# Performance work log

Measured on AMD Instinct MI355X. Metric: run time of the kernel, lower is better.

## Reference

```python
import jax, jax.numpy as jnp
import numpy as np

N_NODES = 100000
N_EDGES = 1600000
N_ETYPES = 3
IN_FEATS = 128
HEADS = 4
OUT_FEATS = 16
EDGE_FEATS = 64
NEG_SLOPE = 0.2


def setup_inputs() -> dict:
    key = jax.random.key(0)
    ks = jax.random.split(key, 10)
    return {
        "x": jax.random.normal(ks[0], (N_NODES, IN_FEATS), jnp.float32),
        "W": jax.random.normal(ks[1], (IN_FEATS, HEADS * OUT_FEATS), jnp.float32) * 0.05,
        "W_e": jax.random.normal(ks[2], (EDGE_FEATS, HEADS * EDGE_FEATS), jnp.float32) * 0.05,
        "attn_l": jax.random.normal(ks[3], (HEADS, OUT_FEATS), jnp.float32) * 0.1,
        "attn_r": jax.random.normal(ks[4], (HEADS, OUT_FEATS), jnp.float32) * 0.1,
        "attn_e": jax.random.normal(ks[5], (HEADS, EDGE_FEATS), jnp.float32) * 0.1,
        "edge_emb": jax.random.normal(ks[6], (N_ETYPES, EDGE_FEATS), jnp.float32),
        "src": jax.random.randint(ks[7], (N_EDGES,), 0, N_NODES, jnp.int32),
        "dst": jax.random.randint(ks[8], (N_EDGES,), 0, N_NODES, jnp.int32),
        "etype": jax.random.randint(ks[9], (N_EDGES,), 0, N_ETYPES, jnp.int32),
    }


def reference(x, W, W_e, attn_l, attn_r, attn_e, edge_emb, src, dst, etype):
    N = x.shape[0]
    H, D = attn_l.shape
    # node projection: [N, H, D]
    feat = (x @ W).reshape(N, H, D)
    # per-node attention halves: [N, H]
    el = jnp.einsum("nhd,hd->nh", feat, attn_l)
    er = jnp.einsum("nhd,hd->nh", feat, attn_r)
    # per-etype edge term: [T, H]
    e_feat = (edge_emb @ W_e).reshape(edge_emb.shape[0], H, -1)
    ee = jnp.einsum("the,he->th", e_feat, attn_e)
    # per-edge pre-softmax score: [E, H]
    s = el[src] + er[dst] + ee[etype]
    s = jnp.where(s > 0, s, NEG_SLOPE * s)  # leaky_relu
    # edge softmax over incoming edges of each dst node (homogeneous graph)
    m = jax.ops.segment_max(s, dst, num_segments=N)
    e = jnp.exp(s - m[dst])
    z = jax.ops.segment_sum(e, dst, num_segments=N)
    a = e / z[dst]  # [E, H]
    # u_mul_e + sum aggregation: [N, H, D]
    msg = feat[src] * a[:, :, None]
    rst = jax.ops.segment_sum(msg, dst, num_segments=N)
    return rst, a
```

## Files before the change

kernel.cpp:

```cpp
#include <hip/hip_runtime.h>
#include <hip/hip_bf16.h>

#define N_NODES   100000
#define N_EDGES   1600000
#define N_ETYPES  3
#define IN_FEATS  128
#define HEADS     4
#define OUT_FEATS 16
#define EDGE_FEATS 64
#define HD        64
#define NEG_SLOPE 0.2f
#define MAXD_LDS  128

#define NBUCK     800
#define NPB       125
#define PBLK      400
#define EPB       4000
#define BCAP      2560

typedef short s16x8 __attribute__((ext_vector_type(8)));
typedef float f32x4 __attribute__((ext_vector_type(4)));

__device__ __forceinline__ short f2bs(float f) {
    __hip_bfloat16 h = __float2bfloat16(f);
    return *reinterpret_cast<short*>(&h);
}

__global__ __launch_bounds__(256) void wt_prep_kernel(
    const float* __restrict__ W, short* __restrict__ WTb)
{
    const int t = blockIdx.x * 256 + threadIdx.x;
    const int k = t >> 6, n = t & 63;
    WTb[n * IN_FEATS + k] = f2bs(W[t]);
}

#define XS_STRIDE 136
__global__ __launch_bounds__(256) void feat_el_er_kernel(
    const float* __restrict__ x,
    const short* __restrict__ WTb,
    const float* __restrict__ attn_l,
    const float* __restrict__ attn_r,
    __hip_bfloat16* __restrict__ featb,
    float* __restrict__ el,
    float* __restrict__ er)
{
    __shared__ short Xs[16 * XS_STRIDE];
    __shared__ short Ws[64 * XS_STRIDE];

    const int t = threadIdx.x;
    const int row0 = blockIdx.x * 16;
    {
        const int r = t >> 4, k0 = (t & 15) * 8;
        const float4* xg = (const float4*)(x + (size_t)(row0 + r) * IN_FEATS + k0);
        const float4 v0 = xg[0], v1 = xg[1];
        s16x8 p;
        p[0] = f2bs(v0.x); p[1] = f2bs(v0.y); p[2] = f2bs(v0.z); p[3] = f2bs(v0.w);
        p[4] = f2bs(v1.x); p[5] = f2bs(v1.y); p[6] = f2bs(v1.z); p[7] = f2bs(v1.w);
        *(s16x8*)&Xs[r * XS_STRIDE + k0] = p;
    }
    {
#pragma unroll
        for (int j = 0; j < 4; ++j) {
            const int u = t + 256 * j;
            const int r = u >> 4, c = (u & 15) * 8;
            *(s16x8*)&Ws[r * XS_STRIDE + c] = *(const s16x8*)(WTb + r * IN_FEATS + c);
        }
    }
    __syncthreads();

    const int w    = t >> 6;
    const int lane = t & 63;
    const int m    = lane & 15;
    const int q    = lane >> 4;

    f32x4 acc = {0.f, 0.f, 0.f, 0.f};
#pragma unroll
    for (int kb = 0; kb < 4; ++kb) {
        const s16x8 af = *(const s16x8*)&Xs[m * XS_STRIDE + kb * 32 + q * 8];
        const s16x8 bf = *(const s16x8*)&Ws[(w * 16 + m) * XS_STRIDE + kb * 32 + q * 8];
        acc = __builtin_amdgcn_mfma_f32_16x16x32_bf16(af, bf, acc, 0, 0, 0);
    }

    const float al = attn_l[w * OUT_FEATS + m];
    const float ar = attn_r[w * OUT_FEATS + m];
#pragma unroll
    for (int r = 0; r < 4; ++r) {
        const int row = row0 + q * 4 + r;
        featb[(size_t)row * HD + w * 16 + m] = __float2bfloat16(acc[r]);
        float cl = acc[r] * al;
        float cr = acc[r] * ar;
#pragma unroll
        for (int msk = 1; msk < 16; msk <<= 1) {
            cl += __shfl_xor(cl, msk, 64);
            cr += __shfl_xor(cr, msk, 64);
        }
        if (m == 0) {
            el[row * HEADS + w] = cl;
            er[row * HEADS + w] = cr;
        }
    }
}

__global__ __launch_bounds__(64) void ee_kernel(
    const float* __restrict__ edge_emb,
    const float* __restrict__ W_e,
    const float* __restrict__ attn_e,
    float* __restrict__ ee)
{
    const int b  = blockIdx.x;
    const int ty = b >> 2;
    const int h  = b & 3;
    const int e  = threadIdx.x;

    float ef = 0.f;
#pragma unroll
    for (int k = 0; k < EDGE_FEATS; ++k)
        ef += edge_emb[ty * EDGE_FEATS + k] *
              W_e[k * (HEADS * EDGE_FEATS) + h * EDGE_FEATS + e];
    float v = ef * attn_e[h * EDGE_FEATS + e];
#pragma unroll
    for (int m = 1; m < 64; m <<= 1) v += __shfl_xor(v, m, 64);
    if (e == 0) ee[ty * HEADS + h] = v;
}

__global__ __launch_bounds__(256) void bucket_hist_kernel(
    const int* __restrict__ dst, int* __restrict__ bhist)
{
    __shared__ int h[NBUCK];
    const int t = threadIdx.x, b = blockIdx.x;
    for (int j = t; j < NBUCK; j += 256) h[j] = 0;
    __syncthreads();
    const int e0 = b * EPB;
    for (int i = t; i < EPB; i += 256)
        atomicAdd(&h[dst[e0 + i] / NPB], 1);
    __syncthreads();
    for (int j = t; j < NBUCK; j += 256) bhist[b * NBUCK + j] = h[j];
}

__global__ __launch_bounds__(256) void bucket_scan1_kernel(
    int* __restrict__ bhist, int* __restrict__ btot)
{
    __shared__ int sh[PBLK];
    const int t = threadIdx.x, j = blockIdx.x;
    const int j0 = t, j1 = t + 256;
    int o0 = 0, o1 = 0;
    if (j0 < PBLK) { o0 = bhist[j0 * NBUCK + j]; sh[j0] = o0; }
    if (j1 < PBLK) { o1 = bhist[j1 * NBUCK + j]; sh[j1] = o1; }
    __syncthreads();
    for (int off = 1; off < PBLK; off <<= 1) {
        int v0 = (j0 >= off && j0 < PBLK) ? sh[j0 - off] : 0;
        int v1 = (j1 >= off && j1 < PBLK) ? sh[j1 - off] : 0;
        __syncthreads();
        if (j0 < PBLK) sh[j0] += v0;
        if (j1 < PBLK) sh[j1] += v1;
        __syncthreads();
    }
    if (j0 < PBLK) bhist[j0 * NBUCK + j] = sh[j0] - o0;
    if (j1 < PBLK) bhist[j1 * NBUCK + j] = sh[j1] - o1;
    if (t == 255) btot[j] = sh[PBLK - 1];
}

__global__ __launch_bounds__(1024) void bucket_scan2_kernel(
    const int* __restrict__ btot, int* __restrict__ bbase)
{
    __shared__ int sh[NBUCK];
    const int t = threadIdx.x;
    int o = 0;
    if (t < NBUCK) { o = btot[t]; sh[t] = o; }
    __syncthreads();
    for (int off = 1; off < NBUCK; off <<= 1) {
        int v = (t >= off && t < NBUCK) ? sh[t - off] : 0;
        __syncthreads();
        if (t < NBUCK) sh[t] += v;
        __syncthreads();
    }
    if (t < NBUCK) bbase[t] = sh[t] - o;
    if (t == NBUCK - 1) bbase[NBUCK] = sh[t];
}

__global__ __launch_bounds__(256) void bucket_scatter_kernel(
    const int* __restrict__ src, const int* __restrict__ dst,
    const int* __restrict__ etype,
    const int* __restrict__ bhist, const int* __restrict__ bbase,
    int2* __restrict__ sc_bucket)
{
    __shared__ int cnt[NBUCK];
    const int t = threadIdx.x, b = blockIdx.x;
    for (int j = t; j < NBUCK; j += 256)
        cnt[j] = bbase[j] + bhist[b * NBUCK + j];
    __syncthreads();
    const int e0 = b * EPB;
    for (int i = t; i < EPB; i += 256) {
        const int e  = e0 + i;
        const int dn = dst[e];
        const int bu = dn / NPB;
        const int ld = dn - bu * NPB;
        const int slot = atomicAdd(&cnt[bu], 1);
        sc_bucket[slot] = make_int2(src[e], e | (etype[e] << 21) | (ld << 23));
    }
}

__global__ __launch_bounds__(256) void bucket_csr_kernel(
    const int2* __restrict__ sc_bucket, const int* __restrict__ bbase,
    int* __restrict__ ptr, int2* __restrict__ sc_csr)
{
    __shared__ int2 sbuf[BCAP];
    __shared__ int sdeg[128];
    __shared__ int scur[128];
    const int t = threadIdx.x, b = blockIdx.x;
    const int lo = bbase[b];
    const int count = bbase[b + 1] - lo;
    const bool staged = (count <= BCAP);

    if (t < 128) sdeg[t] = 0;
    __syncthreads();
    if (staged) {
        for (int i = t; i < count; i += 256) {
            const int2 v = sc_bucket[lo + i];
            sbuf[i] = v;
            atomicAdd(&sdeg[(v.y >> 23) & 0x7F], 1);
        }
    } else {
        for (int i = t; i < count; i += 256)
            atomicAdd(&sdeg[(sc_bucket[lo + i].y >> 23) & 0x7F], 1);
    }
    __syncthreads();
    const int orig = (t < 128) ? sdeg[t] : 0;
    for (int off = 1; off < 128; off <<= 1) {
        const int v = (t < 128 && t >= off) ? sdeg[t - off] : 0;
        __syncthreads();
        if (t < 128) sdeg[t] += v;
        __syncthreads();
    }
    if (t < 128) {
        const int excl = sdeg[t] - orig;
        if (t < NPB) ptr[b * NPB + t] = lo + excl;
        scur[t] = lo + excl;
    }
    if (b == 0 && t == 0) ptr[N_NODES] = N_EDGES;
    __syncthreads();
    if (staged) {
        for (int i = t; i < count; i += 256) {
            const int2 v = sbuf[i];
            const int ld = (v.y >> 23) & 0x7F;
            const int slot = atomicAdd(&scur[ld], 1);
            sc_csr[slot] = make_int2(v.x, (v.y & 0x1FFFFF) | (((v.y >> 21) & 3) << 24));
        }
    } else {
        for (int i = t; i < count; i += 256) {
            const int2 v = sc_bucket[lo + i];
            const int ld = (v.y >> 23) & 0x7F;
            const int slot = atomicAdd(&scur[ld], 1);
            sc_csr[slot] = make_int2(v.x, (v.y & 0x1FFFFF) | (((v.y >> 21) & 3) << 24));
        }
    }
}

__global__ __launch_bounds__(256) void agg_kernel(
    const int2* __restrict__ sc_csr, const int* __restrict__ ptr,
    const float* __restrict__ el, const float* __restrict__ er,
    const float* __restrict__ ee, const __hip_bfloat16* __restrict__ featb,
    float* __restrict__ rst, float* __restrict__ invz)
{
    __shared__ float w_lds[4][MAXD_LDS * HEADS];
    __shared__ int   s_lds[4][MAXD_LDS];
    const int wid  = threadIdx.x >> 6;
    const int lane = threadIdx.x & 63;
    const int n    = blockIdx.x * 4 + wid;

    const int p0  = ptr[n];
    const int deg = ptr[n + 1] - p0;
    float* wl = w_lds[wid];
    int*   sl = s_lds[wid];
    const ushort* fb = (const ushort*)featb;

    if (deg <= MAXD_LDS) {
        const int eo = lane >> 2;
        const int hA = lane & 3;
        const float er_n = er[n * HEADS + hA];
        const float g0 = ee[hA], g1 = ee[HEADS + hA], g2 = ee[2 * HEADS + hA];

        float zacc = 0.f;
        for (int i0 = 0; i0 < deg; i0 += 16) {
            const int idx = i0 + eo;
            float w = 0.f;
            if (idx < deg) {
                const int2 sc = sc_csr[p0 + idx];
                const int ty = sc.y >> 24;
                float s = el[sc.x * HEADS + hA] + er_n +
                          ((ty == 0) ? g0 : ((ty == 1) ? g1 : g2));
                s = s > 0.f ? s : NEG_SLOPE * s;
                w = __expf(s);
                wl[idx * HEADS + hA] = w;
                if (hA == 0) sl[idx] = sc.x;
            }
            zacc += w;
        }
        zacc += __shfl_xor(zacc, 4, 64);
        zacc += __shfl_xor(zacc, 8, 64);
        zacc += __shfl_xor(zacc, 16, 64);
        zacc += __shfl_xor(zacc, 32, 64);
        if (lane < 4)
            invz[n * HEADS + lane] = (deg > 0) ? __frcp_rn(zacc) : 0.f;

        const int q  = lane >> 4;
        const int c  = lane & 15;
        const int hB = c >> 2;
        const float inv_z = (deg > 0) ? __frcp_rn(__shfl(zacc, hB, 64)) : 0.f;

        float a0 = 0.f, a1 = 0.f, a2 = 0.f, a3 = 0.f;
        int i = 0;
        for (; i + 8 <= deg; i += 8) {
            const int idxA = i + q, idxB = i + 4 + q;
            const int sA = sl[idxA], sB = sl[idxB];
            const float wA = wl[idxA * HEADS + hB];
            const float wB = wl[idxB * HEADS + hB];
            const uint2 fA = *(const uint2*)(fb + ((size_t)sA << 6) + (c << 2));
            const uint2 fB = *(const uint2*)(fb + ((size_t)sB << 6) + (c << 2));
            a0 += __uint_as_float(fA.x << 16) * wA + __uint_as_float(fB.x << 16) * wB;
            a1 += __uint_as_float(fA.x & 0xFFFF0000u) * wA + __uint_as_float(fB.x & 0xFFFF0000u) * wB;
            a2 += __uint_as_float(fA.y << 16) * wA + __uint_as_float(fB.y << 16) * wB;
            a3 += __uint_as_float(fA.y & 0xFFFF0000u) * wA + __uint_as_float(fB.y & 0xFFFF0000u) * wB;
        }
        for (; i < deg; i += 4) {
            const int idx = i + q;
            if (idx < deg) {
                const int sA = sl[idx];
                const float wA = wl[idx * HEADS + hB];
                const uint2 fA = *(const uint2*)(fb + ((size_t)sA << 6) + (c << 2));
                a0 += __uint_as_float(fA.x << 16) * wA;
                a1 += __uint_as_float(fA.x & 0xFFFF0000u) * wA;
                a2 += __uint_as_float(fA.y << 16) * wA;
                a3 += __uint_as_float(fA.y & 0xFFFF0000u) * wA;
            }
        }
        a0 += __shfl_xor(a0, 16, 64); a0 += __shfl_xor(a0, 32, 64);
        a1 += __shfl_xor(a1, 16, 64); a1 += __shfl_xor(a1, 32, 64);
        a2 += __shfl_xor(a2, 16, 64); a2 += __shfl_xor(a2, 32, 64);
        a3 += __shfl_xor(a3, 16, 64); a3 += __shfl_xor(a3, 32, 64);
        if (q == 0) {
            f32x4 v = {a0 * inv_z, a1 * inv_z, a2 * inv_z, a3 * inv_z};
            *(f32x4*)(rst + (size_t)n * HD + (c << 2)) = v;
        }
    } else {
        const int hA = lane & 3;
        const int eo = lane >> 2;
        const float er_nA = er[n * HEADS + hA];
        const float a0 = ee[hA], a1 = ee[HEADS + hA], a2 = ee[2 * HEADS + hA];
        float zacc = 0.f;
        for (int base = 0; base < deg; base += 16) {
            const int idx = base + eo;
            if (idx < deg) {
                const int2 sc = sc_csr[p0 + idx];
                const int ty = sc.y >> 24;
                float s = el[sc.x * HEADS + hA] + er_nA + ((ty == 0) ? a0 : ((ty == 1) ? a1 : a2));
                s = s > 0.f ? s : NEG_SLOPE * s;
                zacc += __expf(s);
            }
        }
#pragma unroll
        for (int m = 4; m < 64; m <<= 1) zacc += __shfl_xor(zacc, m, 64);
        if (lane < 4) invz[n * HEADS + lane] = __frcp_rn(zacc);
        const int h = lane >> 4;
        const float inv_z = __frcp_rn(__shfl(zacc, h, 64));
        const float er_n = er[n * HEADS + h];
        const float g0 = ee[h], g1 = ee[HEADS + h], g2 = ee[2 * HEADS + h];
        float racc = 0.f;
        for (int i = 0; i < deg; ++i) {
            const int2 sc = sc_csr[p0 + i];
            const int ty = sc.y >> 24;
            float s = el[sc.x * HEADS + h] + er_n + ((ty == 0) ? g0 : ((ty == 1) ? g1 : g2));
            s = s > 0.f ? s : NEG_SLOPE * s;
            const float a = __expf(s) * inv_z;
            racc += __bfloat162float(featb[(size_t)sc.x * HD + lane]) * a;
        }
        rst[(size_t)n * HD + lane] = racc;
    }
}

__global__ __launch_bounds__(256) void attn_out_kernel(
    const int* __restrict__ src, const int* __restrict__ dst,
    const int* __restrict__ etype,
    const float* __restrict__ el, const float* __restrict__ er,
    const float* __restrict__ ee, const float* __restrict__ invz,
    float* __restrict__ a_out)
{
    const int e = blockIdx.x * 256 + threadIdx.x;
    const int sN = src[e];
    const int dN = dst[e];
    const int ty = etype[e];
    const float4 l4 = *(const float4*)(el + (size_t)sN * HEADS);
    const float4 r4 = *(const float4*)(er + (size_t)dN * HEADS);
    const float4 g4 = *(const float4*)(ee + (size_t)ty * HEADS);
    const float4 iz = *(const float4*)(invz + (size_t)dN * HEADS);
    float4 a;
    float s;
    s = l4.x + r4.x + g4.x; s = s > 0.f ? s : NEG_SLOPE * s; a.x = __expf(s) * iz.x;
    s = l4.y + r4.y + g4.y; s = s > 0.f ? s : NEG_SLOPE * s; a.y = __expf(s) * iz.y;
    s = l4.z + r4.z + g4.z; s = s > 0.f ? s : NEG_SLOPE * s; a.z = __expf(s) * iz.z;
    s = l4.w + r4.w + g4.w; s = s > 0.f ? s : NEG_SLOPE * s; a.w = __expf(s) * iz.w;
    *(float4*)(a_out + (size_t)e * HEADS) = a;
}

extern "C" void kernel_launch(void* const* d_in, const int* in_sizes, int n_in,
                              void* d_out, int out_size, void* d_ws, size_t ws_size,
                              hipStream_t stream)
{
    const float* x        = (const float*)d_in[0];
    const float* W        = (const float*)d_in[1];
    const float* W_e      = (const float*)d_in[2];
    const float* attn_l   = (const float*)d_in[3];
    const float* attn_r   = (const float*)d_in[4];
    const float* attn_e   = (const float*)d_in[5];
    const float* edge_emb = (const float*)d_in[6];
    const int* src   = (const int*)d_in[7];
    const int* dst   = (const int*)d_in[8];
    const int* etype = (const int*)d_in[9];

    float* out     = (float*)d_out;
    float* rst_out = out;
    float* a_out   = out + (size_t)N_NODES * HD;

    char* w = (char*)d_ws;
    __hip_bfloat16* featb = (__hip_bfloat16*)w; w += (size_t)N_NODES * HD * 2;
    float* el    = (float*)w;  w += (size_t)N_NODES * HEADS * 4;
    float* er    = (float*)w;  w += (size_t)N_NODES * HEADS * 4;
    float* ee    = (float*)w;  w += 64;
    int*   ptr   = (int*)w;    w += (size_t)(N_NODES + 4) * 4;
    int*   bhist = (int*)w;    w += (size_t)PBLK * NBUCK * 4;
    int*   btot  = (int*)w;    w += (size_t)NBUCK * 4;
    int*   bbase = (int*)w;    w += (size_t)(NBUCK + 4) * 4;
    short* WTb   = (short*)w;  w += (size_t)HD * IN_FEATS * 2;
    int2*  sc_bucket = (int2*)w; w += (size_t)N_EDGES * 8;
    int2*  sc_csr    = (int2*)w; w += (size_t)N_EDGES * 8;

    float* invz = (float*)sc_bucket;

    wt_prep_kernel<<<(IN_FEATS * HD) / 256, 256, 0, stream>>>(W, WTb);
    feat_el_er_kernel<<<N_NODES / 16, 256, 0, stream>>>(
        x, WTb, attn_l, attn_r, featb, el, er);
    ee_kernel<<<N_ETYPES * HEADS, 64, 0, stream>>>(edge_emb, W_e, attn_e, ee);

    bucket_hist_kernel<<<PBLK, 256, 0, stream>>>(dst, bhist);
    bucket_scan1_kernel<<<NBUCK, 256, 0, stream>>>(bhist, btot);
    bucket_scan2_kernel<<<1, 1024, 0, stream>>>(btot, bbase);
    bucket_scatter_kernel<<<PBLK, 256, 0, stream>>>(src, dst, etype, bhist, bbase, sc_bucket);
    bucket_csr_kernel<<<NBUCK, 256, 0, stream>>>(sc_bucket, bbase, ptr, sc_csr);

    agg_kernel<<<N_NODES / 4, 256, 0, stream>>>(
        sc_csr, ptr, el, er, ee, featb, rst_out, invz);
    attn_out_kernel<<<N_EDGES / 256, 256, 0, stream>>>(
        src, dst, etype, el, er, ee, invz, a_out);
}
```

Before: 289.5 us.

## Pack edge records into 32-bit words, interleave er/invz, widen feature gathers

Edge records in the bucket and CSR arrays shrink from int2 to a single int that packs the source node (17 bits), the edge type (2 bits) and the local destination. The edge id, which was never used, is dropped. This halves the traffic of the scatter, CSR and aggregation stages. er and 1/z are stored interleaved per node, so attn_out reads both with one contiguous access. The aggregation loop now gathers 16 bytes per lane, with 8 lanes per edge row, instead of 8-byte loads. This cuts load instructions but adds an extra shuffle-reduction level and leaves fewer edges in flight per iteration.

```diff
diff --git a/kernel.cpp b/kernel.cpp
--- a/kernel.cpp
+++ b/kernel.cpp
@@ -18,6 +18,7 @@
 #define EPB       4000
 #define BCAP      2560
 
+
 typedef short s16x8 __attribute__((ext_vector_type(8)));
 typedef float f32x4 __attribute__((ext_vector_type(4)));
 
@@ -42,7 +43,7 @@
     const float* __restrict__ attn_r,
     __hip_bfloat16* __restrict__ featb,
     float* __restrict__ el,
-    float* __restrict__ er)
+    float* __restrict__ eriz)
 {
     __shared__ short Xs[16 * XS_STRIDE];
     __shared__ short Ws[64 * XS_STRIDE];
@@ -96,7 +97,7 @@
         }
         if (m == 0) {
             el[row * HEADS + w] = cl;
-            er[row * HEADS + w] = cr;
+            eriz[(size_t)row * 8 + w] = cr;
         }
     }
 }
@@ -182,7 +183,7 @@
     const int* __restrict__ src, const int* __restrict__ dst,
     const int* __restrict__ etype,
     const int* __restrict__ bhist, const int* __restrict__ bbase,
-    int2* __restrict__ sc_bucket)
+    int* __restrict__ sc_bucket)
 {
     __shared__ int cnt[NBUCK];
     const int t = threadIdx.x, b = blockIdx.x;
@@ -196,15 +197,15 @@
         const int bu = dn / NPB;
         const int ld = dn - bu * NPB;
         const int slot = atomicAdd(&cnt[bu], 1);
-        sc_bucket[slot] = make_int2(src[e], e | (etype[e] << 21) | (ld << 23));
+        sc_bucket[slot] = src[e] | (etype[e] << 17) | (ld << 19);
     }
 }
 
 __global__ __launch_bounds__(256) void bucket_csr_kernel(
-    const int2* __restrict__ sc_bucket, const int* __restrict__ bbase,
-    int* __restrict__ ptr, int2* __restrict__ sc_csr)
-{
-    __shared__ int2 sbuf[BCAP];
+    const int* __restrict__ sc_bucket, const int* __restrict__ bbase,
+    int* __restrict__ ptr, int* __restrict__ sc_csr)
+{
+    __shared__ int sbuf[BCAP];
     __shared__ int sdeg[128];
     __shared__ int scur[128];
     const int t = threadIdx.x, b = blockIdx.x;
@@ -216,13 +217,13 @@
     __syncthreads();
     if (staged) {
         for (int i = t; i < count; i += 256) {
-            const int2 v = sc_bucket[lo + i];
+            const int v = sc_bucket[lo + i];
             sbuf[i] = v;
-            atomicAdd(&sdeg[(v.y >> 23) & 0x7F], 1);
+            atomicAdd(&sdeg[(v >> 19) & 0x7F], 1);
         }
     } else {
         for (int i = t; i < count; i += 256)
-            atomicAdd(&sdeg[(sc_bucket[lo + i].y >> 23) & 0x7F], 1);
+            atomicAdd(&sdeg[(sc_bucket[lo + i] >> 19) & 0x7F], 1);
     }
     __syncthreads();
     const int orig = (t < 128) ? sdeg[t] : 0;
@@ -241,26 +242,26 @@
     __syncthreads();
     if (staged) {
         for (int i = t; i < count; i += 256) {
-            const int2 v = sbuf[i];
-            const int ld = (v.y >> 23) & 0x7F;
+            const int v = sbuf[i];
+            const int ld = (v >> 19) & 0x7F;
             const int slot = atomicAdd(&scur[ld], 1);
-            sc_csr[slot] = make_int2(v.x, (v.y & 0x1FFFFF) | (((v.y >> 21) & 3) << 24));
+            sc_csr[slot] = v & 0x7FFFF;
         }
     } else {
         for (int i = t; i < count; i += 256) {
-            const int2 v = sc_bucket[lo + i];
-            const int ld = (v.y >> 23) & 0x7F;
+            const int v = sc_bucket[lo + i];
+            const int ld = (v >> 19) & 0x7F;
             const int slot = atomicAdd(&scur[ld], 1);
-            sc_csr[slot] = make_int2(v.x, (v.y & 0x1FFFFF) | (((v.y >> 21) & 3) << 24));
+            sc_csr[slot] = v & 0x7FFFF;
         }
     }
 }
 
 __global__ __launch_bounds__(256) void agg_kernel(
-    const int2* __restrict__ sc_csr, const int* __restrict__ ptr,
-    const float* __restrict__ el, const float* __restrict__ er,
+    const int* __restrict__ sc_csr, const int* __restrict__ ptr,
+    const float* __restrict__ el, float* __restrict__ eriz,
     const float* __restrict__ ee, const __hip_bfloat16* __restrict__ featb,
-    float* __restrict__ rst, float* __restrict__ invz)
+    float* __restrict__ rst)
 {
     __shared__ float w_lds[4][MAXD_LDS * HEADS];
     __shared__ int   s_lds[4][MAXD_LDS];
@@ -277,102 +278,115 @@
     if (deg <= MAXD_LDS) {
         const int eo = lane >> 2;
         const int hA = lane & 3;
-        const float er_n = er[n * HEADS + hA];
+        const float er_n = eriz[(size_t)n * 8 + hA];
         const float g0 = ee[hA], g1 = ee[HEADS + hA], g2 = ee[2 * HEADS + hA];
 
         float zacc = 0.f;
         for (int i0 = 0; i0 < deg; i0 += 16) {
             const int idx = i0 + eo;
-            float w = 0.f;
             if (idx < deg) {
-                const int2 sc = sc_csr[p0 + idx];
-                const int ty = sc.y >> 24;
-                float s = el[sc.x * HEADS + hA] + er_n +
+                const int v  = sc_csr[p0 + idx];
+                const int sn = v & 0x1FFFF;
+                const int ty = v >> 17;
+                float s = el[sn * HEADS + hA] + er_n +
                           ((ty == 0) ? g0 : ((ty == 1) ? g1 : g2));
                 s = s > 0.f ? s : NEG_SLOPE * s;
-                w = __expf(s);
+                const float w = __expf(s);
                 wl[idx * HEADS + hA] = w;
-                if (hA == 0) sl[idx] = sc.x;
+                if (hA == 0) sl[idx] = sn;
+                zacc += w;
             }
-            zacc += w;
         }
         zacc += __shfl_xor(zacc, 4, 64);
         zacc += __shfl_xor(zacc, 8, 64);
         zacc += __shfl_xor(zacc, 16, 64);
         zacc += __shfl_xor(zacc, 32, 64);
         if (lane < 4)
-            invz[n * HEADS + lane] = (deg > 0) ? __frcp_rn(zacc) : 0.f;
-
-        const int q  = lane >> 4;
-        const int c  = lane & 15;
-        const int hB = c >> 2;
-        const float inv_z = (deg > 0) ? __frcp_rn(__shfl(zacc, hB, 64)) : 0.f;
+            eriz[(size_t)n * 8 + 4 + lane] = (deg > 0) ? __frcp_rn(zacc) : 0.f;
+
+        const int q8 = lane >> 3;
+        const int c8 = lane & 7;
+        const int h8 = c8 >> 1;
+        const float inv_z = (deg > 0) ? __frcp_rn(__shfl(zacc, h8, 64)) : 0.f;
 
         float a0 = 0.f, a1 = 0.f, a2 = 0.f, a3 = 0.f;
+        float a4 = 0.f, a5 = 0.f, a6 = 0.f, a7 = 0.f;
         int i = 0;
         for (; i + 8 <= deg; i += 8) {
-            const int idxA = i + q, idxB = i + 4 + q;
-            const int sA = sl[idxA], sB = sl[idxB];
-            const float wA = wl[idxA * HEADS + hB];
-            const float wB = wl[idxB * HEADS + hB];
-            const uint2 fA = *(const uint2*)(fb + ((size_t)sA << 6) + (c << 2));
-            const uint2 fB = *(const uint2*)(fb + ((size_t)sB << 6) + (c << 2));
-            a0 += __uint_as_float(fA.x << 16) * wA + __uint_as_float(fB.x << 16) * wB;
-            a1 += __uint_as_float(fA.x & 0xFFFF0000u) * wA + __uint_as_float(fB.x & 0xFFFF0000u) * wB;
-            a2 += __uint_as_float(fA.y << 16) * wA + __uint_as_float(fB.y << 16) * wB;
-            a3 += __uint_as_float(fA.y & 0xFFFF0000u) * wA + __uint_as_float(fB.y & 0xFFFF0000u) * wB;
-        }
-        for (; i < deg; i += 4) {
-            const int idx = i + q;
-            if (idx < deg) {
-                const int sA = sl[idx];
-                const float wA = wl[idx * HEADS + hB];
-                const uint2 fA = *(const uint2*)(fb + ((size_t)sA << 6) + (c << 2));
-                a0 += __uint_as_float(fA.x << 16) * wA;
-                a1 += __uint_as_float(fA.x & 0xFFFF0000u) * wA;
-                a2 += __uint_as_float(fA.y << 16) * wA;
-                a3 += __uint_as_float(fA.y & 0xFFFF0000u) * wA;
-            }
-        }
-        a0 += __shfl_xor(a0, 16, 64); a0 += __shfl_xor(a0, 32, 64);
-        a1 += __shfl_xor(a1, 16, 64); a1 += __shfl_xor(a1, 32, 64);
-        a2 += __shfl_xor(a2, 16, 64); a2 += __shfl_xor(a2, 32, 64);
-        a3 += __shfl_xor(a3, 16, 64); a3 += __shfl_xor(a3, 32, 64);
-        if (q == 0) {
-            f32x4 v = {a0 * inv_z, a1 * inv_z, a2 * inv_z, a3 * inv_z};
-            *(f32x4*)(rst + (size_t)n * HD + (c << 2)) = v;
+            const int idx = i + q8;
+            const int sA = sl[idx];
+            const float wA = wl[idx * HEADS + h8];
+            const uint4 fA = *(const uint4*)(fb + ((size_t)sA << 6) + (c8 << 3));
+            a0 += __uint_as_float(fA.x << 16) * wA;
+            a1 += __uint_as_float(fA.x & 0xFFFF0000u) * wA;
+            a2 += __uint_as_float(fA.y << 16) * wA;
+            a3 += __uint_as_float(fA.y & 0xFFFF0000u) * wA;
+            a4 += __uint_as_float(fA.z << 16) * wA;
+            a5 += __uint_as_float(fA.z & 0xFFFF0000u) * wA;
+            a6 += __uint_as_float(fA.w << 16) * wA;
+            a7 += __uint_as_float(fA.w & 0xFFFF0000u) * wA;
+        }
+        if (i + q8 < deg) {
+            const int idx = i + q8;
+            const int sA = sl[idx];
+            const float wA = wl[idx * HEADS + h8];
+            const uint4 fA = *(const uint4*)(fb + ((size_t)sA << 6) + (c8 << 3));
+            a0 += __uint_as_float(fA.x << 16) * wA;
+            a1 += __uint_as_float(fA.x & 0xFFFF0000u) * wA;
+            a2 += __uint_as_float(fA.y << 16) * wA;
+            a3 += __uint_as_float(fA.y & 0xFFFF0000u) * wA;
+            a4 += __uint_as_float(fA.z << 16) * wA;
+            a5 += __uint_as_float(fA.z & 0xFFFF0000u) * wA;
+            a6 += __uint_as_float(fA.w << 16) * wA;
+            a7 += __uint_as_float(fA.w & 0xFFFF0000u) * wA;
+        }
+        a0 += __shfl_xor(a0, 8, 64); a0 += __shfl_xor(a0, 16, 64); a0 += __shfl_xor(a0, 32, 64);
+        a1 += __shfl_xor(a1, 8, 64); a1 += __shfl_xor(a1, 16, 64); a1 += __shfl_xor(a1, 32, 64);
+        a2 += __shfl_xor(a2, 8, 64); a2 += __shfl_xor(a2, 16, 64); a2 += __shfl_xor(a2, 32, 64);
+        a3 += __shfl_xor(a3, 8, 64); a3 += __shfl_xor(a3, 16, 64); a3 += __shfl_xor(a3, 32, 64);
+        a4 += __shfl_xor(a4, 8, 64); a4 += __shfl_xor(a4, 16, 64); a4 += __shfl_xor(a4, 32, 64);
+        a5 += __shfl_xor(a5, 8, 64); a5 += __shfl_xor(a5, 16, 64); a5 += __shfl_xor(a5, 32, 64);
+        a6 += __shfl_xor(a6, 8, 64); a6 += __shfl_xor(a6, 16, 64); a6 += __shfl_xor(a6, 32, 64);
+        a7 += __shfl_xor(a7, 8, 64); a7 += __shfl_xor(a7, 16, 64); a7 += __shfl_xor(a7, 32, 64);
+        if (q8 == 0) {
+            f32x4 v0 = {a0 * inv_z, a1 * inv_z, a2 * inv_z, a3 * inv_z};
+            f32x4 v1 = {a4 * inv_z, a5 * inv_z, a6 * inv_z, a7 * inv_z};
+            *(f32x4*)(rst + (size_t)n * HD + (c8 << 3))     = v0;
+            *(f32x4*)(rst + (size_t)n * HD + (c8 << 3) + 4) = v1;
         }
     } else {
         const int hA = lane & 3;
         const int eo = lane >> 2;
-        const float er_nA = er[n * HEADS + hA];
+        const float er_nA = eriz[(size_t)n * 8 + hA];
         const float a0 = ee[hA], a1 = ee[HEADS + hA], a2 = ee[2 * HEADS + hA];
         float zacc = 0.f;
         for (int base = 0; base < deg; base += 16) {
             const int idx = base + eo;
             if (idx < deg) {
-                const int2 sc = sc_csr[p0 + idx];
-                const int ty = sc.y >> 24;
-                float s = el[sc.x * HEADS + hA] + er_nA + ((ty == 0) ? a0 : ((ty == 1) ? a1 : a2));
+                const int v  = sc_csr[p0 + idx];
+                const int sn = v & 0x1FFFF;
+                const int ty = v >> 17;
+                float s = el[sn * HEADS + hA] + er_nA + ((ty == 0) ? a0 : ((ty == 1) ? a1 : a2));
                 s = s > 0.f ? s : NEG_SLOPE * s;
                 zacc += __expf(s);
             }
         }
 #pragma unroll
         for (int m = 4; m < 64; m <<= 1) zacc += __shfl_xor(zacc, m, 64);
-        if (lane < 4) invz[n * HEADS + lane] = __frcp_rn(zacc);
+        if (lane < 4) eriz[(size_t)n * 8 + 4 + lane] = __frcp_rn(zacc);
         const int h = lane >> 4;
         const float inv_z = __frcp_rn(__shfl(zacc, h, 64));
-        const float er_n = er[n * HEADS + h];
+        const float er_n = eriz[(size_t)n * 8 + h];
         const float g0 = ee[h], g1 = ee[HEADS + h], g2 = ee[2 * HEADS + h];
         float racc = 0.f;
         for (int i = 0; i < deg; ++i) {
-            const int2 sc = sc_csr[p0 + i];
-            const int ty = sc.y >> 24;
-            float s = el[sc.x * HEADS + h] + er_n + ((ty == 0) ? g0 : ((ty == 1) ? g1 : g2));
+            const int v  = sc_csr[p0 + i];
+            const int sn = v & 0x1FFFF;
+            const int ty = v >> 17;
+            float s = el[sn * HEADS + h] + er_n + ((ty == 0) ? g0 : ((ty == 1) ? g1 : g2));
             s = s > 0.f ? s : NEG_SLOPE * s;
             const float a = __expf(s) * inv_z;
-            racc += __bfloat162float(featb[(size_t)sc.x * HD + lane]) * a;
+            racc += __bfloat162float(featb[(size_t)sn * HD + lane]) * a;
         }
         rst[(size_t)n * HD + lane] = racc;
     }
@@ -381,8 +395,8 @@
 __global__ __launch_bounds__(256) void attn_out_kernel(
     const int* __restrict__ src, const int* __restrict__ dst,
     const int* __restrict__ etype,
-    const float* __restrict__ el, const float* __restrict__ er,
-    const float* __restrict__ ee, const float* __restrict__ invz,
+    const float* __restrict__ el, const float* __restrict__ eriz,
+    const float* __restrict__ ee,
     float* __restrict__ a_out)
 {
     const int e = blockIdx.x * 256 + threadIdx.x;
@@ -390,9 +404,9 @@
     const int dN = dst[e];
     const int ty = etype[e];
     const float4 l4 = *(const float4*)(el + (size_t)sN * HEADS);
-    const float4 r4 = *(const float4*)(er + (size_t)dN * HEADS);
+    const float4 r4 = *(const float4*)(eriz + (size_t)dN * 8);
+    const float4 iz = *(const float4*)(eriz + (size_t)dN * 8 + 4);
     const float4 g4 = *(const float4*)(ee + (size_t)ty * HEADS);
-    const float4 iz = *(const float4*)(invz + (size_t)dN * HEADS);
     float4 a;
     float s;
     s = l4.x + r4.x + g4.x; s = s > 0.f ? s : NEG_SLOPE * s; a.x = __expf(s) * iz.x;
@@ -424,21 +438,19 @@
     char* w = (char*)d_ws;
     __hip_bfloat16* featb = (__hip_bfloat16*)w; w += (size_t)N_NODES * HD * 2;
     float* el    = (float*)w;  w += (size_t)N_NODES * HEADS * 4;
-    float* er    = (float*)w;  w += (size_t)N_NODES * HEADS * 4;
+    float* eriz  = (float*)w;  w += (size_t)N_NODES * 8 * 4;
     float* ee    = (float*)w;  w += 64;
     int*   ptr   = (int*)w;    w += (size_t)(N_NODES + 4) * 4;
     int*   bhist = (int*)w;    w += (size_t)PBLK * NBUCK * 4;
     int*   btot  = (int*)w;    w += (size_t)NBUCK * 4;
     int*   bbase = (int*)w;    w += (size_t)(NBUCK + 4) * 4;
     short* WTb   = (short*)w;  w += (size_t)HD * IN_FEATS * 2;
-    int2*  sc_bucket = (int2*)w; w += (size_t)N_EDGES * 8;
-    int2*  sc_csr    = (int2*)w; w += (size_t)N_EDGES * 8;
-
-    float* invz = (float*)sc_bucket;
+    int*   sc_bucket = (int*)w; w += (size_t)N_EDGES * 4;
+    int*   sc_csr    = (int*)w; w += (size_t)N_EDGES * 4;
 
     wt_prep_kernel<<<(IN_FEATS * HD) / 256, 256, 0, stream>>>(W, WTb);
     feat_el_er_kernel<<<N_NODES / 16, 256, 0, stream>>>(
-        x, WTb, attn_l, attn_r, featb, el, er);
+        x, WTb, attn_l, attn_r, featb, el, eriz);
     ee_kernel<<<N_ETYPES * HEADS, 64, 0, stream>>>(edge_emb, W_e, attn_e, ee);
 
     bucket_hist_kernel<<<PBLK, 256, 0, stream>>>(dst, bhist);
@@ -448,7 +460,7 @@
     bucket_csr_kernel<<<NBUCK, 256, 0, stream>>>(sc_bucket, bbase, ptr, sc_csr);
 
     agg_kernel<<<N_NODES / 4, 256, 0, stream>>>(
-        sc_csr, ptr, el, er, ee, featb, rst_out, invz);
+        sc_csr, ptr, el, eriz, ee, featb, rst_out);
     attn_out_kernel<<<N_EDGES / 256, 256, 0, stream>>>(
-        src, dst, etype, el, er, ee, invz, a_out);
-}
+        src, dst, etype, el, eriz, ee, a_out);
+}
```

New measurement: 287.9 us. No clear change (-0.5%).
